# Kernel tuning notes

Hardware: AMD Instinct MI355X
Metric: run time of the kernel (lower is better)

Reference implementation:

```python
import jax, jax.numpy as jnp
import numpy as np

SCORE_THR = 0.5
IOU_THR = 0.5
N_ANCHORS = 8400  # standard YOLO 640x640 anchor count


def setup_inputs() -> dict:
    key = jax.random.key(0)
    # [1, 5, N]: channels are (cx, cy, w, h, person_conf); uniform keeps boxes/scores in [0,1)
    yolo_raw_out = jax.random.uniform(key, (1, 5, N_ANCHORS), dtype=jnp.float32)
    return {"yolo_raw_out": yolo_raw_out}


def _pairwise_iou(b):
    # b: [N,4] xyxy
    area = (b[:, 2] - b[:, 0]) * (b[:, 3] - b[:, 1])          # [N]
    lt = jnp.maximum(b[:, None, :2], b[None, :, :2])          # [N,N,2]
    rb = jnp.minimum(b[:, None, 2:], b[None, :, 2:])          # [N,N,2]
    wh = jnp.clip(rb - lt, 0.0)
    inter = wh[..., 0] * wh[..., 1]                           # [N,N]
    union = area[:, None] + area[None, :] - inter
    return inter / jnp.maximum(union, 1e-9)


def reference(yolo_raw_out):
    # permute(0,2,1).squeeze(0) -> [N,5]
    raw = yolo_raw_out[0].T
    cx, cy, w, h = raw[:, 0], raw[:, 1], raw[:, 2], raw[:, 3]
    scores = raw[:, 4]
    # cxcywh -> xyxy (torchvision.ops.box_convert)
    xyxy = jnp.stack([cx - w / 2, cy - h / 2, cx + w / 2, cy + h / 2], axis=-1)

    valid = scores >= SCORE_THR
    # sort by score descending; invalid boxes pushed to the end
    order = jnp.argsort(-jnp.where(valid, scores, -jnp.inf))
    sb = xyxy[order]          # [N,4] sorted boxes
    ss = scores[order]        # [N]
    sv = valid[order]         # [N] score-threshold mask

    iou = _pairwise_iou(sb)   # [N,N]
    n = ss.shape[0]
    idx = jnp.arange(n)

    # Greedy NMS: in score order, an active (kept, valid) box suppresses all
    # lower-scored boxes with IoU > threshold. Faithful to torchvision.ops.nms.
    def step(keep, i):
        active = keep[i]
        suppress = (iou[i] > IOU_THR) & (idx > i) & active
        return keep & ~suppress, None

    keep, _ = jax.lax.scan(step, sv, idx)

    # Fixed-shape output: kept rows carry (x1,y1,x2,y2,score); suppressed/filtered rows zeroed.
    out = jnp.concatenate([sb, ss[:, None]], axis=1) * keep[:, None].astype(ss.dtype)
    return out
```

## Files before the change

kernel.cpp:

```cpp
#include <hip/hip_runtime.h>
#include <cstdint>

#define N_ANCH 8400
#define CBLK 132
#define SCORE_THR 0.5f

typedef unsigned long long u64;
typedef unsigned int u32;

__device__ __forceinline__ u64 sort_key(float s, int idx) {
  u32 k32 = (s >= SCORE_THR) ? ~__float_as_uint(s) : 0xFFFFFFFFu;
  return ((u64)k32 << 32) | (u32)idx;
}

__device__ __forceinline__ u64 rfl64(u64 v) {
  u32 lo = (u32)__builtin_amdgcn_readfirstlane((int)(u32)v);
  u32 hi = (u32)__builtin_amdgcn_readfirstlane((int)(u32)(v >> 32));
  return ((u64)hi << 32) | lo;
}

__global__ void __launch_bounds__(256) rank_kernel(const float* __restrict__ raw,
                                                   float4* __restrict__ sbox,
                                                   float* __restrict__ sscore) {
  #pragma clang fp contract(off)
  int tid = blockIdx.x * 256 + threadIdx.x;
  int row = tid >> 6, lane = tid & 63;
  if (row >= N_ANCH) return;
  float si = raw[4 * N_ANCH + row];
  u64 ki = sort_key(si, row);
  int cnt = 0;
  for (int j = lane; j < N_ANCH; j += 64) {
    float sj = raw[4 * N_ANCH + j];
    cnt += (sort_key(sj, j) < ki) ? 1 : 0;
  }
  #pragma unroll
  for (int d = 1; d < 64; d <<= 1) cnt += __shfl_xor(cnt, d, 64);
  if (lane == 0) {
    float cx = raw[row], cy = raw[N_ANCH + row];
    float w = raw[2 * N_ANCH + row], h = raw[3 * N_ANCH + row];
    float hw = w * 0.5f, hh = h * 0.5f;
    sbox[cnt] = make_float4(cx - hw, cy - hh, cx + hw, cy + hh);
    sscore[cnt] = si;
  }
}

__global__ void __launch_bounds__(256) mask_kernel(const float4* __restrict__ sbox,
                                                   const float* __restrict__ sscore,
                                                   u64* __restrict__ mask) {
  #pragma clang fp contract(off)
  int cb = blockIdx.x;
  int i0 = blockIdx.y * 256;
  if (cb + 3 < (i0 >> 6)) return;
  if (!(sscore[i0] >= SCORE_THR)) return;
  if (!(sscore[cb * 64] >= SCORE_THR)) return;
  int t = threadIdx.x;
  __shared__ float4 cbox[64];
  __shared__ float carea[64];
  int j0 = cb * 64;
  if (t < 64) {
    int j = j0 + t;
    float4 bj = (j < N_ANCH) ? sbox[j] : make_float4(0.f, 0.f, 0.f, 0.f);
    cbox[t] = bj;
    carea[t] = (bj.z - bj.x) * (bj.w - bj.y);
  }
  __syncthreads();
  int i = i0 + t;
  if (i >= N_ANCH) return;
  float4 bi = sbox[i];
  float ai = (bi.z - bi.x) * (bi.w - bi.y);
  u64 wHi = 0, wLo = 0;
  for (int jj = 0; jj < 64; ++jj) {
    int jg = j0 + jj;
    float4 bb = cbox[jj];
    float ltx = fmaxf(bi.x, bb.x), lty = fmaxf(bi.y, bb.y);
    float rbx = fminf(bi.z, bb.z), rby = fminf(bi.w, bb.w);
    float wx = fmaxf(rbx - ltx, 0.f), wy = fmaxf(rby - lty, 0.f);
    float inter = wx * wy;
    float uni = (ai + carea[jj]) - inter;
    float iou = inter / fmaxf(uni, 1e-9f);
    bool sup = (iou > 0.5f) && (jg < N_ANCH);
    wHi |= (u64)(sup && (jg > i)) << jj;
    wLo |= (u64)(sup && (jg < i)) << jj;
  }
  mask[(u64)i * CBLK + cb] = (cb > (i >> 6)) ? wHi : wLo;
}

__global__ void __launch_bounds__(512, 1) nms_kernel(const float4* __restrict__ sbox,
                                                     const float* __restrict__ sscore,
                                                     const u64* __restrict__ mask,
                                                     float* __restrict__ out) {
  __shared__ u64 keepw[CBLK + 2];
  __shared__ u64 rem[CBLK + 2];
  int tid = threadIdx.x;
  int wave = tid >> 6, lane = tid & 63;

  float s0 = sscore[lane * 132];
  u64 pb = __ballot(s0 >= SCORE_THR);
  int cnt1 = (int)__popcll(pb);
  int n_valid = 0;
  if (cnt1 > 0) {
    int a = (cnt1 - 1) * 132 + 1;
    int i1 = a + 3 * lane;
    float t1 = (i1 + 0 < N_ANCH) ? sscore[i1 + 0] : -1.f;
    float t2 = (i1 + 1 < N_ANCH) ? sscore[i1 + 1] : -1.f;
    float t3 = (i1 + 2 < N_ANCH) ? sscore[i1 + 2] : -1.f;
    u64 q1 = __ballot(t1 >= SCORE_THR);
    u64 q2 = __ballot(t2 >= SCORE_THR);
    u64 q3 = __ballot(t3 >= SCORE_THR);
    n_valid = a + (int)__popcll(q1) + (int)__popcll(q2) + (int)__popcll(q3);
  }
  int VB = (n_valid + 63) >> 6;
  int NT = (VB + 1) >> 1;

  for (int b = tid; b < CBLK + 2; b += 512) { keepw[b] = 0; rem[b] = 0; }

  int rs = (wave - 1) * 19;
  int nr = 128 - rs; if (nr > 19) nr = 19;
  u64 tl[19], th[19];
  auto issue_tiles = [&](int u) {
    int base = 2 * u + 4;
    if (base >= VB) return;
    int cL = base + lane;
    bool okL = (cL < VB);
    const u64* pr = mask + (u64)(128 * u + rs) * CBLK;
    #pragma unroll
    for (int r = 0; r < 19; ++r) {
      bool rok = (r < nr);
      tl[r] = (rok && okL) ? pr[(u64)r * CBLK + cL] : 0ull;
    }
    if (base + 64 < VB) {
      int cH = cL + 64;
      bool okH = (cH < VB);
      #pragma unroll
      for (int r = 0; r < 19; ++r) {
        bool rok = (r < nr);
        th[r] = (rok && okH) ? pr[(u64)r * CBLK + cH] : 0ull;
      }
    }
  };

  u64 cA=0,cB=0,cC=0,cD0=0,cD1=0,cE0=0,cE1=0;
  u64 nA=0,nB=0,nC=0,nD0=0,nD1=0,nE0=0,nE1=0;
  auto load_w0 = [&](int T2, u64&A,u64&B,u64&C,u64&D0,u64&D1,u64&E0,u64&E1) {
    int b0 = 2 * T2, b1 = b0 + 1;
    int r0 = b0 * 64 + lane;
    int r1 = b1 * 64 + lane; if (r1 > N_ANCH - 1) r1 = N_ANCH - 1;
    int r2 = (b0 + 2) * 64 + lane; if (r2 > N_ANCH - 1) r2 = N_ANCH - 1;
    int r3 = (b0 + 3) * 64 + lane; if (r3 > N_ANCH - 1) r3 = N_ANCH - 1;
    bool ok1 = (b1 < VB), ok2 = (b0 + 2 < VB), ok3 = (b0 + 3 < VB);
    const u64* p0 = mask + (u64)r0 * CBLK;
    const u64* p1 = mask + (u64)r1 * CBLK;
    const u64* p2 = mask + (u64)r2 * CBLK;
    const u64* p3 = mask + (u64)r3 * CBLK;
    A  = p0[b0];
    B  = ok1 ? p1[b0] : 0ull;
    C  = ok1 ? p1[b1] : 0ull;
    D0 = ok2 ? p2[b0] : 0ull;
    D1 = ok2 ? p2[b1] : 0ull;
    E0 = ok3 ? p3[b0] : 0ull;
    E1 = ok3 ? p3[b1] : 0ull;
  };

  u64 carry0 = 0, carry1 = 0;

  if (wave == 0 && NT > 0) load_w0(0, cA,cB,cC,cD0,cD1,cE0,cE1);

  for (int T = 0; T < NT; ++T) {
    asm volatile("s_waitcnt lgkmcnt(0)\ns_barrier" ::: "memory");

    if (wave == 0) {
      __builtin_amdgcn_s_setprio(1);
      int b0 = 2 * T, b1 = b0 + 1;
      u64 rb0 = rem[b0], rb1 = rem[b1];
      if (T > 0) { cA=nA; cB=nB; cC=nC; cD0=nD0; cD1=nD1; cE0=nE0; cE1=nE1; }
      if (T + 1 < NT) load_w0(T + 1, nA,nB,nC,nD0,nD1,nE0,nE1);

      u64 remb0 = rfl64(rb0 | carry0);
      u64 remb1 = rfl64(rb1 | carry1);
      int remn0 = n_valid - b0 * 64;
      int remn1 = remn0 - 64;
      u64 vm0 = (remn0 >= 64) ? ~0ull : ((1ull << remn0) - 1ull);
      u64 vm1 = (remn1 >= 64) ? ~0ull
              : ((remn1 <= 0) ? 0ull : ((1ull << remn1) - 1ull));
      u64 act0 = vm0 & ~remb0;
      u64 act1 = vm1 & ~remb1;

      u64 U = act0, K0 = 0;
      while (U) {
        u64 covered = __ballot((cA & U) != 0ull);
        u64 nk = U & ~covered;
        u64 supp = __ballot((cA & nk) != 0ull);
        K0 |= nk;
        U &= ~(nk | supp);
      }
      u64 kw0 = K0;

      u64 s01 = __ballot((cB & kw0) != 0ull);
      u64 U1 = act1 & ~s01, K1 = 0;
      while (U1) {
        u64 covered = __ballot((cC & U1) != 0ull);
        u64 nk = U1 & ~covered;
        u64 supp = __ballot((cC & nk) != 0ull);
        K1 |= nk;
        U1 &= ~(nk | supp);
      }
      u64 kw1 = K1;

      if (lane == 0) { keepw[b0] = kw0; keepw[b1] = kw1; }

      carry0 = __ballot(((cD0 & kw0) | (cD1 & kw1)) != 0ull);
      carry1 = __ballot(((cE0 & kw0) | (cE1 & kw1)) != 0ull);
      __builtin_amdgcn_s_setprio(0);
    } else {
      if (T > 0) {
        int u = T - 1;
        int base = 2 * u + 4;
        if (base < VB) {
          u64 kws0 = rfl64(keepw[2 * u]);
          u64 kws1 = rfl64(keepw[2 * u + 1]);
          u64 accL = 0;
          #pragma unroll
          for (int r = 0; r < 19; ++r) {
            int rr = rs + r;
            u64 bit = (rr < 64) ? (kws0 >> rr) : (kws1 >> (rr - 64));
            u64 sm = (u64)0 - (bit & 1ull);
            accL |= tl[r] & sm;
          }
          int cL = base + lane;
          if (cL < VB && accL) atomicOr((unsigned long long*)&rem[cL], accL);
          if (base + 64 < VB) {
            u64 accH = 0;
            #pragma unroll
            for (int r = 0; r < 19; ++r) {
              int rr = rs + r;
              u64 bit = (rr < 64) ? (kws0 >> rr) : (kws1 >> (rr - 64));
              u64 sm = (u64)0 - (bit & 1ull);
              accH |= th[r] & sm;
            }
            int cH = base + 64 + lane;
            if (cH < VB && accH) atomicOr((unsigned long long*)&rem[cH], accH);
          }
        }
      }
      if (T + 1 < NT) issue_tiles(T);
    }
  }
  __syncthreads();

  for (int r2 = tid; r2 < N_ANCH; r2 += 512) {
    u64 kv = keepw[r2 >> 6];
    bool kp = (kv >> (r2 & 63)) & 1ull;
    float4 b4 = sbox[r2];
    float sc = sscore[r2];
    float* o = out + r2 * 5;
    o[0] = kp ? b4.x : 0.f;
    o[1] = kp ? b4.y : 0.f;
    o[2] = kp ? b4.z : 0.f;
    o[3] = kp ? b4.w : 0.f;
    o[4] = kp ? sc : 0.f;
  }
}

extern "C" void kernel_launch(void* const* d_in, const int* in_sizes, int n_in,
                              void* d_out, int out_size, void* d_ws, size_t ws_size,
                              hipStream_t stream) {
  const float* raw = (const float*)d_in[0];
  float* out = (float*)d_out;
  char* ws = (char*)d_ws;
  float4* sbox = (float4*)ws;
  float* sscore = (float*)(ws + 8448 * 16);
  u64* mask = (u64*)(ws + 8448 * 16 + 8448 * 4);

  rank_kernel<<<2100, 256, 0, stream>>>(raw, sbox, sscore);
  mask_kernel<<<dim3(CBLK, 33), 256, 0, stream>>>(sbox, sscore, mask);
  nms_kernel<<<1, 512, 0, stream>>>(sbox, sscore, mask, out);
}
```

Measured before the change: 155.1 us.

## Deepen NMS carry window to four blocks and load only kept mask rows

Wave 0 now handles direct suppression carry for the next four column blocks instead of two. A two-stage delayed carry lets the helper waves handle columns from base+6 onward with a one-step lag. Helper waves now issue mask loads only for rows whose keep bit is already known, rather than prefetching every row and masking afterwards. This removes wasted global loads, and the extra slack gives those loads time to finish before the OR-reduction. The mask kernel's diagonal band widens to cb+5 so the extra carry blocks are computed. The cost is more registers in wave 0 and a more intricate carry schedule that has to stay correct.

```diff
diff --git a/kernel.cpp b/kernel.cpp
--- a/kernel.cpp
+++ b/kernel.cpp
@@ -50,7 +50,7 @@
   #pragma clang fp contract(off)
   int cb = blockIdx.x;
   int i0 = blockIdx.y * 256;
-  if (cb + 3 < (i0 >> 6)) return;
+  if (cb + 5 < (i0 >> 6)) return;
   if (!(sscore[i0] >= SCORE_THR)) return;
   if (!(sscore[cb * 64] >= SCORE_THR)) return;
   int t = threadIdx.x;
@@ -117,53 +117,41 @@
   int rs = (wave - 1) * 19;
   int nr = 128 - rs; if (nr > 19) nr = 19;
   u64 tl[19], th[19];
-  auto issue_tiles = [&](int u) {
-    int base = 2 * u + 4;
-    if (base >= VB) return;
-    int cL = base + lane;
-    bool okL = (cL < VB);
-    const u64* pr = mask + (u64)(128 * u + rs) * CBLK;
-    #pragma unroll
-    for (int r = 0; r < 19; ++r) {
-      bool rok = (r < nr);
-      tl[r] = (rok && okL) ? pr[(u64)r * CBLK + cL] : 0ull;
-    }
-    if (base + 64 < VB) {
-      int cH = cL + 64;
-      bool okH = (cH < VB);
-      #pragma unroll
-      for (int r = 0; r < 19; ++r) {
-        bool rok = (r < nr);
-        th[r] = (rok && okH) ? pr[(u64)r * CBLK + cH] : 0ull;
-      }
-    }
-  };
-
-  u64 cA=0,cB=0,cC=0,cD0=0,cD1=0,cE0=0,cE1=0;
-  u64 nA=0,nB=0,nC=0,nD0=0,nD1=0,nE0=0,nE1=0;
-  auto load_w0 = [&](int T2, u64&A,u64&B,u64&C,u64&D0,u64&D1,u64&E0,u64&E1) {
+
+  u64 cA=0,cB=0,cC=0,cD0=0,cD1=0,cE0=0,cE1=0,cF0=0,cF1=0,cG0=0,cG1=0;
+  u64 nA=0,nB=0,nC=0,nD0=0,nD1=0,nE0=0,nE1=0,nF0=0,nF1=0,nG0=0,nG1=0;
+  auto load_w0 = [&](int T2, u64&A,u64&B,u64&C,u64&D0,u64&D1,u64&E0,u64&E1,
+                     u64&F0,u64&F1,u64&G0,u64&G1) {
     int b0 = 2 * T2, b1 = b0 + 1;
     int r0 = b0 * 64 + lane;
     int r1 = b1 * 64 + lane; if (r1 > N_ANCH - 1) r1 = N_ANCH - 1;
     int r2 = (b0 + 2) * 64 + lane; if (r2 > N_ANCH - 1) r2 = N_ANCH - 1;
     int r3 = (b0 + 3) * 64 + lane; if (r3 > N_ANCH - 1) r3 = N_ANCH - 1;
+    int r4 = (b0 + 4) * 64 + lane; if (r4 > N_ANCH - 1) r4 = N_ANCH - 1;
+    int r5 = (b0 + 5) * 64 + lane; if (r5 > N_ANCH - 1) r5 = N_ANCH - 1;
     bool ok1 = (b1 < VB), ok2 = (b0 + 2 < VB), ok3 = (b0 + 3 < VB);
+    bool ok4 = (b0 + 4 < VB), ok5 = (b0 + 5 < VB);
     const u64* p0 = mask + (u64)r0 * CBLK;
     const u64* p1 = mask + (u64)r1 * CBLK;
     const u64* p2 = mask + (u64)r2 * CBLK;
     const u64* p3 = mask + (u64)r3 * CBLK;
+    const u64* p4 = mask + (u64)r4 * CBLK;
+    const u64* p5 = mask + (u64)r5 * CBLK;
     A  = p0[b0];
     B  = ok1 ? p1[b0] : 0ull;
     C  = ok1 ? p1[b1] : 0ull;
-    D0 = ok2 ? p2[b0] : 0ull;
-    D1 = ok2 ? p2[b1] : 0ull;
-    E0 = ok3 ? p3[b0] : 0ull;
-    E1 = ok3 ? p3[b1] : 0ull;
+    D0 = ok2 ? p2[b0] : 0ull;  D1 = ok2 ? p2[b1] : 0ull;
+    E0 = ok3 ? p3[b0] : 0ull;  E1 = ok3 ? p3[b1] : 0ull;
+    F0 = ok4 ? p4[b0] : 0ull;  F1 = ok4 ? p4[b1] : 0ull;
+    G0 = ok5 ? p5[b0] : 0ull;  G1 = ok5 ? p5[b1] : 0ull;
   };
 
-  u64 carry0 = 0, carry1 = 0;
-
-  if (wave == 0 && NT > 0) load_w0(0, cA,cB,cC,cD0,cD1,cE0,cE1);
+  u64 p0c = 0, p1c = 0;
+  u64 q0c = 0, q1c = 0;
+  u64 qn0 = 0, qn1 = 0;
+
+  if (wave == 0 && NT > 0)
+    load_w0(0, cA,cB,cC,cD0,cD1,cE0,cE1,cF0,cF1,cG0,cG1);
 
   for (int T = 0; T < NT; ++T) {
     asm volatile("s_waitcnt lgkmcnt(0)\ns_barrier" ::: "memory");
@@ -172,11 +160,13 @@
       __builtin_amdgcn_s_setprio(1);
       int b0 = 2 * T, b1 = b0 + 1;
       u64 rb0 = rem[b0], rb1 = rem[b1];
-      if (T > 0) { cA=nA; cB=nB; cC=nC; cD0=nD0; cD1=nD1; cE0=nE0; cE1=nE1; }
-      if (T + 1 < NT) load_w0(T + 1, nA,nB,nC,nD0,nD1,nE0,nE1);
-
-      u64 remb0 = rfl64(rb0 | carry0);
-      u64 remb1 = rfl64(rb1 | carry1);
+      if (T > 0) { cA=nA; cB=nB; cC=nC; cD0=nD0; cD1=nD1; cE0=nE0; cE1=nE1;
+                   cF0=nF0; cF1=nF1; cG0=nG0; cG1=nG1; }
+      if (T + 1 < NT)
+        load_w0(T + 1, nA,nB,nC,nD0,nD1,nE0,nE1,nF0,nF1,nG0,nG1);
+
+      u64 remb0 = rfl64(rb0) | p0c | q0c;
+      u64 remb1 = rfl64(rb1) | p1c | q1c;
       int remn0 = n_valid - b0 * 64;
       int remn1 = remn0 - 64;
       u64 vm0 = (remn0 >= 64) ? ~0ull : ((1ull << remn0) - 1ull);
@@ -208,41 +198,62 @@
 
       if (lane == 0) { keepw[b0] = kw0; keepw[b1] = kw1; }
 
-      carry0 = __ballot(((cD0 & kw0) | (cD1 & kw1)) != 0ull);
-      carry1 = __ballot(((cE0 & kw0) | (cE1 & kw1)) != 0ull);
+      u64 f2 = __ballot(((cD0 & kw0) | (cD1 & kw1)) != 0ull);
+      u64 f3 = __ballot(((cE0 & kw0) | (cE1 & kw1)) != 0ull);
+      u64 f4 = __ballot(((cF0 & kw0) | (cF1 & kw1)) != 0ull);
+      u64 f5 = __ballot(((cG0 & kw0) | (cG1 & kw1)) != 0ull);
+      p0c = f2; p1c = f3;
+      q0c = qn0; q1c = qn1;
+      qn0 = f4; qn1 = f5;
       __builtin_amdgcn_s_setprio(0);
     } else {
-      if (T > 0) {
+      if (T >= 2) {
+        int u = T - 2;
+        int base = 2 * u + 6;
+        if (base < VB) {
+          u64 acc = 0;
+          #pragma unroll
+          for (int r = 0; r < 19; ++r) acc |= tl[r];
+          int cL = base + lane;
+          if (cL < VB && acc) atomicOr((unsigned long long*)&rem[cL], acc);
+          if (base + 64 < VB) {
+            u64 acc2 = 0;
+            #pragma unroll
+            for (int r = 0; r < 19; ++r) acc2 |= th[r];
+            int cH = base + 64 + lane;
+            if (cH < VB && acc2) atomicOr((unsigned long long*)&rem[cH], acc2);
+          }
+        }
+      }
+      if (T >= 1 && T + 1 < NT) {
         int u = T - 1;
-        int base = 2 * u + 4;
+        int base = 2 * u + 6;
         if (base < VB) {
           u64 kws0 = rfl64(keepw[2 * u]);
           u64 kws1 = rfl64(keepw[2 * u + 1]);
-          u64 accL = 0;
+          int cL = base + lane;
+          bool okL = (cL < VB);
+          const u64* pr = mask + (u64)(128 * u + rs) * CBLK;
           #pragma unroll
           for (int r = 0; r < 19; ++r) {
             int rr = rs + r;
-            u64 bit = (rr < 64) ? (kws0 >> rr) : (kws1 >> (rr - 64));
-            u64 sm = (u64)0 - (bit & 1ull);
-            accL |= tl[r] & sm;
+            u64 kb = (rr < 64) ? (kws0 >> rr) : (kws1 >> (rr - 64));
+            bool rok = (r < nr) && ((kb & 1ull) != 0ull);
+            tl[r] = (rok && okL) ? pr[(u64)r * CBLK + cL] : 0ull;
           }
-          int cL = base + lane;
-          if (cL < VB && accL) atomicOr((unsigned long long*)&rem[cL], accL);
           if (base + 64 < VB) {
-            u64 accH = 0;
+            int cH = cL + 64;
+            bool okH = (cH < VB);
             #pragma unroll
             for (int r = 0; r < 19; ++r) {
               int rr = rs + r;
-              u64 bit = (rr < 64) ? (kws0 >> rr) : (kws1 >> (rr - 64));
-              u64 sm = (u64)0 - (bit & 1ull);
-              accH |= th[r] & sm;
+              u64 kb = (rr < 64) ? (kws0 >> rr) : (kws1 >> (rr - 64));
+              bool rok = (r < nr) && ((kb & 1ull) != 0ull);
+              th[r] = (rok && okH) ? pr[(u64)r * CBLK + cH] : 0ull;
             }
-            int cH = base + 64 + lane;
-            if (cH < VB && accH) atomicOr((unsigned long long*)&rem[cH], accH);
           }
         }
       }
-      if (T + 1 < NT) issue_tiles(T);
     }
   }
   __syncthreads();
```

Result: faster. 147.4 us (-4.9%).
